# Performance work log

Measured on AMD Instinct MI355X. Metric: run time of the kernel, lower is better.

Reference implementation:

```python
import jax, jax.numpy as jnp
import numpy as np

R, K = 16, 64  # rel_size (heads), key_size (head dim)
LN_EPS = 1e-5


def apply_rope(x, pos):
    # pos: [B,S,1,K], halves are sin/cos; x: [B,S,R,K]
    sin, cos = jnp.split(pos, 2, axis=-1)
    x0, x1 = jnp.split(x, 2, axis=-1)
    return jnp.concatenate([x0 * cos - x1 * sin, x0 * sin + x1 * cos], axis=-1)


def setup_inputs() -> dict:
    key = jax.random.key(0)
    ks = jax.random.split(key, 6)
    B, S, H = 2, 2048, 1024
    x = jax.random.normal(ks[0], (B, S, H), dtype=jnp.float32)
    pos = jax.random.uniform(ks[1], (B, S, 1, K), dtype=jnp.float32)
    W_qkv = jax.random.normal(ks[2], (H, R * K * 3), dtype=jnp.float32) * (H ** -0.5)
    b_qkv = jax.random.normal(ks[3], (R * K * 3,), dtype=jnp.float32) * 0.02
    W_out = jax.random.normal(ks[4], (R * K, H), dtype=jnp.float32) * ((R * K) ** -0.5)
    b_out = jax.random.normal(ks[5], (H,), dtype=jnp.float32) * 0.02
    ln_g = jnp.ones((H,), dtype=jnp.float32)
    ln_b = jnp.zeros((H,), dtype=jnp.float32)
    return {"x": x, "pos": pos, "W_qkv": W_qkv, "b_qkv": b_qkv,
            "W_out": W_out, "b_out": b_out, "ln_g": ln_g, "ln_b": ln_b}


def reference(x, pos, W_qkv, b_qkv, W_out, b_out, ln_g, ln_b):
    B, S, H = x.shape
    qkv = (x @ W_qkv + b_qkv).reshape(B, S, R, 3 * K)
    q, k, v = jnp.split(qkv, 3, axis=-1)  # each [B,S,R,K]
    k = k / jnp.linalg.norm(k, axis=-1, keepdims=True)
    q = apply_rope(q, pos)
    k = apply_rope(k, pos)
    # SDPA with scale=1 (as in the original call)
    scores = jnp.einsum('bqhd,bkhd->bhqk', q, k)
    attn = jax.nn.softmax(scores, axis=-1)
    ctx = jnp.einsum('bhqk,bkhd->bqhd', attn, v).reshape(B, S, R * K)
    postx = ctx @ W_out + b_out
    y = x + postx
    mu = jnp.mean(y, axis=-1, keepdims=True)
    var = jnp.mean(jnp.square(y - mu), axis=-1, keepdims=True)
    return (y - mu) * jax.lax.rsqrt(var + LN_EPS) * ln_g + ln_b
```

## Files before the change

### kernel.cpp

```cpp
#include <hip/hip_runtime.h>


#define B_   2
#define S_   2048
#define H_   1024
#define R_   16
#define BS_  (B_*S_)
#define NQKV 3072
#define LOG2E 1.44269504088896f

typedef float    floatx4 __attribute__((ext_vector_type(4)));
typedef _Float16 half8   __attribute__((ext_vector_type(8)));
typedef _Float16 half4   __attribute__((ext_vector_type(4)));
typedef __fp16   fp16x2  __attribute__((ext_vector_type(2)));

#if __has_builtin(__builtin_amdgcn_exp2f)
#define EXP2(x) __builtin_amdgcn_exp2f(x)
#else
#define EXP2(x) exp2f(x)
#endif

__device__ __forceinline__ void gl_lds16(const _Float16* g, _Float16* l) {
    __builtin_amdgcn_global_load_lds(
        (const __attribute__((address_space(1))) unsigned int*)g,
        (__attribute__((address_space(3))) unsigned int*)l, 16, 0, 0);
}

__global__ __launch_bounds__(256) void cast_f16_kernel(
    const float* __restrict__ in, _Float16* __restrict__ out, int n)
{
    int i = (blockIdx.x * 256 + threadIdx.x) * 4;
    if (i >= n) return;
    float4 v = *(const float4*)(in + i);
    half4 h;
    h.x = (_Float16)v.x; h.y = (_Float16)v.y; h.z = (_Float16)v.z; h.w = (_Float16)v.w;
    *(half4*)(out + i) = h;
}

__global__ __launch_bounds__(256) void transpose_cast_f16(
    const float* __restrict__ in, _Float16* __restrict__ out, int rows, int cols)
{
    __shared__ float tile[32][33];
    int bx = blockIdx.x * 32;
    int by = blockIdx.y * 32;
    int tx = threadIdx.x & 31, ty = threadIdx.x >> 5;
#pragma unroll
    for (int i = 0; i < 32; i += 8)
        tile[ty + i][tx] = in[(size_t)(by + ty + i) * cols + bx + tx];
    __syncthreads();
#pragma unroll
    for (int i = 0; i < 32; i += 8)
        out[(size_t)(bx + ty + i) * rows + by + tx] = (_Float16)tile[tx][ty + i];
}

template <bool F16OUT>
__global__ __launch_bounds__(256) void gemm_f16_mfma(
    const _Float16* __restrict__ A, const _Float16* __restrict__ Bt,
    const float* __restrict__ bias, const float* __restrict__ resid,
    float* __restrict__ Cf, _Float16* __restrict__ Ch, int M, int N, int Kd)
{
    __shared__ _Float16 Als[2][4096];
    __shared__ _Float16 Bls[2][4096];
    int tid  = threadIdx.x;
    int lane = tid & 63, w = tid >> 6;
    int wr = w >> 1, wc = w & 1;
    int fr = lane & 15, fq = lane >> 4;
    int m0 = blockIdx.y * 128, n0 = blockIdx.x * 128;

    floatx4 acc[4][4] = {};

    const _Float16* ga[2]; const _Float16* gb[2];
    int loff[2];
#pragma unroll
    for (int i2 = 0; i2 < 2; ++i2) {
        int ch = 2 * w + i2;
        int row = ch * 16 + (lane >> 2), col = (lane & 3) * 8;
        ga[i2] = A  + (size_t)(m0 + row) * Kd + col;
        gb[i2] = Bt + (size_t)(n0 + row) * Kd + col;
        loff[i2] = ch * 512;
    }

    int nIter = Kd >> 5;
#pragma unroll
    for (int i2 = 0; i2 < 2; ++i2) {
        gl_lds16(ga[i2], &Als[0][loff[i2]]);
        gl_lds16(gb[i2], &Bls[0][loff[i2]]);
    }

    for (int it = 0; it < nIter; ++it) {
        int cur = it & 1;
        __syncthreads();
        if (it + 1 < nIter) {
            int k1 = (it + 1) << 5;
#pragma unroll
            for (int i2 = 0; i2 < 2; ++i2) {
                gl_lds16(ga[i2] + k1, &Als[cur ^ 1][loff[i2]]);
                gl_lds16(gb[i2] + k1, &Bls[cur ^ 1][loff[i2]]);
            }
        }
        const _Float16* Ab = Als[cur];
        const _Float16* Bb = Bls[cur];
        half8 af[4], bf[4];
#pragma unroll
        for (int i = 0; i < 4; ++i)
            af[i] = *(const half8*)(Ab + (wr * 64 + i * 16 + fr) * 32 + fq * 8);
#pragma unroll
        for (int j = 0; j < 4; ++j)
            bf[j] = *(const half8*)(Bb + (wc * 64 + j * 16 + fr) * 32 + fq * 8);
#pragma unroll
        for (int i = 0; i < 4; ++i)
#pragma unroll
            for (int j = 0; j < 4; ++j)
                acc[i][j] = __builtin_amdgcn_mfma_f32_16x16x32_f16(
                    af[i], bf[j], acc[i][j], 0, 0, 0);
    }

#pragma unroll
    for (int i = 0; i < 4; ++i)
#pragma unroll
        for (int j = 0; j < 4; ++j)
#pragma unroll
            for (int r2 = 0; r2 < 4; ++r2) {
                int row = m0 + wr * 64 + i * 16 + fq * 4 + r2;
                int col = n0 + wc * 64 + j * 16 + fr;
                float v = acc[i][j][r2] + bias[col];
                if constexpr (F16OUT) {
                    Ch[(size_t)row * N + col] = (_Float16)v;
                } else {
                    if (resid) v += resid[(size_t)row * N + col];
                    Cf[(size_t)row * N + col] = v;
                }
            }
}

__global__ __launch_bounds__(256) void rope_kernel(
    const _Float16* __restrict__ qkvh, const float* __restrict__ pos,
    _Float16* __restrict__ qt, _Float16* __restrict__ kt)
{
    int task = blockIdx.x * 4 + (threadIdx.x >> 6);
    int lane = threadIdx.x & 63;
    int r = task & 15, bs = task >> 4;
    int b = bs >> 11, s = bs & 2047;

    const _Float16* base = qkvh + (size_t)bs * NQKV + r * 192;
    float qv = (float)base[lane];
    float kv = (float)base[64 + lane];

    float ss = kv * kv;
#pragma unroll
    for (int off = 32; off > 0; off >>= 1) ss += __shfl_xor(ss, off);
    kv *= rsqrtf(ss);

    int j = lane & 31;
    float sn = pos[(size_t)bs * 64 + j];
    float cs = pos[(size_t)bs * 64 + 32 + j];
    float qp = __shfl_xor(qv, 32);
    float kp = __shfl_xor(kv, 32);
    float qo, ko;
    if (lane < 32) { qo = qv * cs - qp * sn; ko = kv * cs - kp * sn; }
    else           { qo = qp * sn + qv * cs; ko = kp * sn + kv * cs; }

    size_t oidx = ((size_t)(b * 16 + r) * S_ + s) * 64 + lane;
    qt[oidx] = (_Float16)(qo * LOG2E);
    kt[oidx] = (_Float16)ko;
}

__global__ __launch_bounds__(256) void vtrans_kernel(
    const _Float16* __restrict__ qkvh, _Float16* __restrict__ vt2)
{
    __shared__ float tile[64][65];
    int head = blockIdx.x, tau = blockIdx.y;
    int s0 = tau * 64;
    int b = head >> 4, rh = head & 15;
    int tx = threadIdx.x & 63, ty = threadIdx.x >> 6;
#pragma unroll
    for (int si = ty; si < 64; si += 4)
        tile[si][tx] = (float)qkvh[(size_t)(b * S_ + s0 + si) * NQKV + rh * 192 + 128 + tx];
    __syncthreads();
    int P = tx;
    int op = P >> 3;
    int hi = (P >> 2) & 1, lo = P & 3;
#pragma unroll
    for (int d = ty; d < 64; d += 4) {
        int ol = op ^ (d & 7);
        int key = 32 * (ol >> 2) + 16 * hi + 4 * (ol & 3) + lo;
        vt2[(((size_t)head * 32 + tau) * 64 + d) * 64 + P] = (_Float16)tile[key][d];
    }
}

__global__ __launch_bounds__(256) void attn_mfma_kernel(
    const _Float16* __restrict__ qt, const _Float16* __restrict__ kt,
    const _Float16* __restrict__ vt2, _Float16* __restrict__ ctx)
{
    __shared__ _Float16 Kls[64 * 64];
    __shared__ _Float16 Vls[64 * 64];

    int head = blockIdx.x, q0 = blockIdx.y * 128;
    int b = head >> 4, rh = head & 15;
    int tid = threadIdx.x, lane = tid & 63, w = tid >> 6;
    int g = lane >> 4, c = lane & 15;

    half8 qf[2][2];
    float mL[2], l_s[2] = {0.f, 0.f};
#pragma unroll
    for (int qg = 0; qg < 2; ++qg) {
        const _Float16* qp =
            qt + ((size_t)head * S_ + q0 + w * 32 + qg * 16 + c) * 64 + 8 * g;
        qf[qg][0] = *(const half8*)qp;
        qf[qg][1] = *(const half8*)(qp + 32);
        float qq = 0.f;
#pragma unroll
        for (int i = 0; i < 8; ++i) {
            float a = (float)qf[qg][0][i], b2 = (float)qf[qg][1][i];
            qq += a * a + b2 * b2;
        }
        qq += __shfl_xor(qq, 16);
        qq += __shfl_xor(qq, 32);
        mL[qg] = sqrtf(qq);
    }

    floatx4 o_acc[2][4] = {};

    const _Float16* kg[2]; const _Float16* vg[2];
    _Float16 *kl_[2], *vl_[2];
#pragma unroll
    for (int i2 = 0; i2 < 2; ++i2) {
        int ch = 2 * w + i2;
        int krow = ch * 8 + (lane >> 3);
        int koct = (lane & 7) ^ (lane >> 3);
        kg[i2] = kt + ((size_t)head * S_ + krow) * 64 + koct * 8;
        kl_[i2] = Kls + ch * 512;
        vg[i2] = vt2 + ((size_t)head * 32) * 4096 + ch * 512 + lane * 8;
        vl_[i2] = Vls + ch * 512;
    }

    int co = c & 7;

    for (int j0 = 0; j0 < S_; j0 += 64) {
        __syncthreads();
#pragma unroll
        for (int i2 = 0; i2 < 2; ++i2) {
            gl_lds16(kg[i2] + (size_t)j0 * 64, kl_[i2]);
            gl_lds16(vg[i2] + (size_t)(j0 >> 6) * 4096, vl_[i2]);
        }
        __syncthreads();

        half8 kfr[8];
#pragma unroll
        for (int t = 0; t < 4; ++t) {
            const _Float16* krow = Kls + (16 * t + c) * 64;
            kfr[2 * t]     = *(const half8*)(krow + ((g) ^ co) * 8);
            kfr[2 * t + 1] = *(const half8*)(krow + ((4 + g) ^ co) * 8);
        }

        union { half8 v; fp16x2 h2[4]; } pf[2][2];
#pragma unroll
        for (int qg = 0; qg < 2; ++qg) {
            floatx4 sacc[4];
#pragma unroll
            for (int t = 0; t < 4; ++t) {
                floatx4 z = {};
                z = __builtin_amdgcn_mfma_f32_16x16x32_f16(
                    kfr[2 * t], qf[qg][0], z, 0, 0, 0);
                z = __builtin_amdgcn_mfma_f32_16x16x32_f16(
                    kfr[2 * t + 1], qf[qg][1], z, 0, 0, 0);
                sacc[t] = z;
            }
            float mLq = mL[qg], ps = 0.f;
#pragma unroll
            for (int t = 0; t < 4; ++t)
#pragma unroll
                for (int r = 0; r < 4; ++r) {
                    float p = EXP2(sacc[t][r] - mLq);
                    sacc[t][r] = p;
                    ps += p;
                }
            l_s[qg] += ps;
            pf[qg][0].h2[0] = __builtin_amdgcn_cvt_pkrtz(sacc[0][0], sacc[0][1]);
            pf[qg][0].h2[1] = __builtin_amdgcn_cvt_pkrtz(sacc[0][2], sacc[0][3]);
            pf[qg][0].h2[2] = __builtin_amdgcn_cvt_pkrtz(sacc[1][0], sacc[1][1]);
            pf[qg][0].h2[3] = __builtin_amdgcn_cvt_pkrtz(sacc[1][2], sacc[1][3]);
            pf[qg][1].h2[0] = __builtin_amdgcn_cvt_pkrtz(sacc[2][0], sacc[2][1]);
            pf[qg][1].h2[1] = __builtin_amdgcn_cvt_pkrtz(sacc[2][2], sacc[2][3]);
            pf[qg][1].h2[2] = __builtin_amdgcn_cvt_pkrtz(sacc[3][0], sacc[3][1]);
            pf[qg][1].h2[3] = __builtin_amdgcn_cvt_pkrtz(sacc[3][2], sacc[3][3]);
        }

#pragma unroll
        for (int t = 0; t < 4; ++t) {
            const _Float16* vrow = Vls + (16 * t + c) * 64;
            half8 v0 = *(const half8*)(vrow + ((g) ^ co) * 8);
            half8 v1 = *(const half8*)(vrow + ((4 + g) ^ co) * 8);
#pragma unroll
            for (int qg = 0; qg < 2; ++qg) {
                o_acc[qg][t] = __builtin_amdgcn_mfma_f32_16x16x32_f16(
                    v0, pf[qg][0].v, o_acc[qg][t], 0, 0, 0);
                o_acc[qg][t] = __builtin_amdgcn_mfma_f32_16x16x32_f16(
                    v1, pf[qg][1].v, o_acc[qg][t], 0, 0, 0);
            }
        }
    }

#pragma unroll
    for (int qg = 0; qg < 2; ++qg) {
        float lt = l_s[qg];
        lt += __shfl_xor(lt, 16);
        lt += __shfl_xor(lt, 32);
        float inv = 1.f / lt;
        size_t rowbase =
            ((size_t)(b * S_ + q0 + w * 32 + qg * 16 + c)) * 1024 + rh * 64;
#pragma unroll
        for (int t = 0; t < 4; ++t) {
            union { half4 v; fp16x2 h2[2]; } e;
            e.h2[0] = __builtin_amdgcn_cvt_pkrtz(o_acc[qg][t][0] * inv,
                                                 o_acc[qg][t][1] * inv);
            e.h2[1] = __builtin_amdgcn_cvt_pkrtz(o_acc[qg][t][2] * inv,
                                                 o_acc[qg][t][3] * inv);
            *(half4*)(ctx + rowbase + 16 * t + 4 * g) = e.v;
        }
    }
}

__global__ __launch_bounds__(256) void ln_kernel(
    float* __restrict__ y, const float* __restrict__ g, const float* __restrict__ bb)
{
    int row = blockIdx.x, tid = threadIdx.x;
    float* p = y + (size_t)row * 1024;
    float4 v = ((const float4*)p)[tid];
    float sum = v.x + v.y + v.z + v.w;
    float sq  = v.x*v.x + v.y*v.y + v.z*v.z + v.w*v.w;
#pragma unroll
    for (int off = 32; off > 0; off >>= 1) {
        sum += __shfl_xor(sum, off);
        sq  += __shfl_xor(sq,  off);
    }
    __shared__ float rs[4], rq[4];
    int w = tid >> 6;
    if ((tid & 63) == 0) { rs[w] = sum; rq[w] = sq; }
    __syncthreads();
    sum = rs[0] + rs[1] + rs[2] + rs[3];
    sq  = rq[0] + rq[1] + rq[2] + rq[3];
    float mean = sum * (1.f / 1024.f);
    float var  = sq * (1.f / 1024.f) - mean * mean;
    float inv  = rsqrtf(var + 1e-5f);
    float4 gv = ((const float4*)g)[tid];
    float4 bv = ((const float4*)bb)[tid];
    v.x = (v.x - mean) * inv * gv.x + bv.x;
    v.y = (v.y - mean) * inv * gv.y + bv.y;
    v.z = (v.z - mean) * inv * gv.z + bv.z;
    v.w = (v.w - mean) * inv * gv.w + bv.w;
    ((float4*)p)[tid] = v;
}

extern "C" void kernel_launch(void* const* d_in, const int* in_sizes, int n_in,
                              void* d_out, int out_size, void* d_ws, size_t ws_size,
                              hipStream_t stream)
{
    const float* x     = (const float*)d_in[0];
    const float* pos   = (const float*)d_in[1];
    const float* W_qkv = (const float*)d_in[2];
    const float* b_qkv = (const float*)d_in[3];
    const float* W_out = (const float*)d_in[4];
    const float* b_out = (const float*)d_in[5];
    const float* ln_g  = (const float*)d_in[6];
    const float* ln_b  = (const float*)d_in[7];
    float* out = (float*)d_out;

    char* ws = (char*)d_ws;
    _Float16* x_h    = (_Float16*)(ws);
    _Float16* wqkv_t = (_Float16*)(ws + ((size_t)8  << 20));
    _Float16* wout_t = (_Float16*)(ws + ((size_t)14 << 20));
    _Float16* qkvh   = (_Float16*)(ws + ((size_t)16 << 20));
    _Float16* qt_h   = (_Float16*)(ws + ((size_t)40 << 20));
    _Float16* kt_h   = (_Float16*)(ws + ((size_t)48 << 20));
    _Float16* vt2_h  = (_Float16*)(ws + ((size_t)56 << 20));
    _Float16* ctx_h  = (_Float16*)(ws + ((size_t)64 << 20));

    cast_f16_kernel<<<4096, 256, 0, stream>>>(x, x_h, BS_ * H_);
    transpose_cast_f16<<<dim3(96, 32), 256, 0, stream>>>(W_qkv, wqkv_t, H_, NQKV);
    transpose_cast_f16<<<dim3(32, 32), 256, 0, stream>>>(W_out, wout_t, H_, H_);

    gemm_f16_mfma<true><<<dim3(NQKV / 128, BS_ / 128), 256, 0, stream>>>(
        x_h, wqkv_t, b_qkv, nullptr, nullptr, qkvh, BS_, NQKV, H_);

    rope_kernel<<<BS_ * R_ / 4, 256, 0, stream>>>(qkvh, pos, qt_h, kt_h);
    vtrans_kernel<<<dim3(32, 32), 256, 0, stream>>>(qkvh, vt2_h);

    attn_mfma_kernel<<<dim3(32, 16), 256, 0, stream>>>(qt_h, kt_h, vt2_h, ctx_h);

    gemm_f16_mfma<false><<<dim3(H_ / 128, BS_ / 128), 256, 0, stream>>>(
        ctx_h, wout_t, b_out, x, out, nullptr, BS_, H_, H_);

    ln_kernel<<<BS_, 256, 0, stream>>>(out, ln_g, ln_b);
}
```

Baseline: 232.4 us.

## Merge prep kernels into fewer launches and fold max subtraction into MFMA init

Combines the x cast and the two weight transpose-casts into one launch, and merges the RoPE/k-normalisation kernel with the V transpose kernel so each block handles both for one head and sequence tile. In attention, the running max is negated and used as the MFMA accumulator's initial value, which removes a subtraction per score before exp2. The intent is to cut launch overhead and per-element ALU work. The tradeoff is that the fused RoPE loop runs serially, 16 rows per wave, inside fewer blocks, which may reduce parallelism for that stage.

```diff
diff --git a/kernel.cpp b/kernel.cpp
--- a/kernel.cpp
+++ b/kernel.cpp
@@ -14,11 +14,15 @@
 typedef _Float16 half4   __attribute__((ext_vector_type(4)));
 typedef __fp16   fp16x2  __attribute__((ext_vector_type(2)));
 
+__device__ __forceinline__ float exp2_raw(float x) {
 #if __has_builtin(__builtin_amdgcn_exp2f)
-#define EXP2(x) __builtin_amdgcn_exp2f(x)
+    return __builtin_amdgcn_exp2f(x);
 #else
-#define EXP2(x) exp2f(x)
+    float r;
+    asm("v_exp_f32 %0, %1\n\ts_nop 0" : "=v"(r) : "v"(x));
+    return r;
 #endif
+}
 
 __device__ __forceinline__ void gl_lds16(const _Float16* g, _Float16* l) {
     __builtin_amdgcn_global_load_lds(
@@ -26,31 +30,41 @@
         (__attribute__((address_space(3))) unsigned int*)l, 16, 0, 0);
 }
 
-__global__ __launch_bounds__(256) void cast_f16_kernel(
-    const float* __restrict__ in, _Float16* __restrict__ out, int n)
-{
-    int i = (blockIdx.x * 256 + threadIdx.x) * 4;
-    if (i >= n) return;
-    float4 v = *(const float4*)(in + i);
-    half4 h;
-    h.x = (_Float16)v.x; h.y = (_Float16)v.y; h.z = (_Float16)v.z; h.w = (_Float16)v.w;
-    *(half4*)(out + i) = h;
-}
-
-__global__ __launch_bounds__(256) void transpose_cast_f16(
-    const float* __restrict__ in, _Float16* __restrict__ out, int rows, int cols)
+__global__ __launch_bounds__(256) void prep0_kernel(
+    const float* __restrict__ x, _Float16* __restrict__ x_h,
+    const float* __restrict__ W_qkv, _Float16* __restrict__ wqkv_t,
+    const float* __restrict__ W_out, _Float16* __restrict__ wout_t)
 {
     __shared__ float tile[32][33];
-    int bx = blockIdx.x * 32;
-    int by = blockIdx.y * 32;
-    int tx = threadIdx.x & 31, ty = threadIdx.x >> 5;
+    int bid = blockIdx.x, tid = threadIdx.x;
+    if (bid < 4096) {
+        int i = bid * 1024 + tid * 4;
+        float4 v = *(const float4*)(x + i);
+        half4 h;
+        h.x = (_Float16)v.x; h.y = (_Float16)v.y;
+        h.z = (_Float16)v.z; h.w = (_Float16)v.w;
+        *(half4*)(x_h + i) = h;
+        return;
+    }
+    const float* in; _Float16* out; int rows, cols, bx, by;
+    if (bid < 7168) {
+        int t = bid - 4096;
+        in = W_qkv; out = wqkv_t; rows = H_; cols = NQKV;
+        bx = t % 96; by = t / 96;
+    } else {
+        int t = bid - 7168;
+        in = W_out; out = wout_t; rows = H_; cols = H_;
+        bx = t & 31; by = t >> 5;
+    }
+    int cx = bx * 32, ry = by * 32;
+    int tx = tid & 31, ty = tid >> 5;
 #pragma unroll
     for (int i = 0; i < 32; i += 8)
-        tile[ty + i][tx] = in[(size_t)(by + ty + i) * cols + bx + tx];
+        tile[ty + i][tx] = in[(size_t)(ry + ty + i) * cols + cx + tx];
     __syncthreads();
 #pragma unroll
     for (int i = 0; i < 32; i += 8)
-        out[(size_t)(bx + ty + i) * rows + by + tx] = (_Float16)tile[tx][ty + i];
+        out[(size_t)(cx + ty + i) * rows + ry + tx] = (_Float16)tile[tx][ty + i];
 }
 
 template <bool F16OUT>
@@ -133,58 +147,58 @@
             }
 }
 
-__global__ __launch_bounds__(256) void rope_kernel(
+__global__ __launch_bounds__(256) void prep1_kernel(
     const _Float16* __restrict__ qkvh, const float* __restrict__ pos,
-    _Float16* __restrict__ qt, _Float16* __restrict__ kt)
-{
-    int task = blockIdx.x * 4 + (threadIdx.x >> 6);
-    int lane = threadIdx.x & 63;
-    int r = task & 15, bs = task >> 4;
-    int b = bs >> 11, s = bs & 2047;
-
-    const _Float16* base = qkvh + (size_t)bs * NQKV + r * 192;
-    float qv = (float)base[lane];
-    float kv = (float)base[64 + lane];
-
-    float ss = kv * kv;
-#pragma unroll
-    for (int off = 32; off > 0; off >>= 1) ss += __shfl_xor(ss, off);
-    kv *= rsqrtf(ss);
-
-    int j = lane & 31;
-    float sn = pos[(size_t)bs * 64 + j];
-    float cs = pos[(size_t)bs * 64 + 32 + j];
-    float qp = __shfl_xor(qv, 32);
-    float kp = __shfl_xor(kv, 32);
-    float qo, ko;
-    if (lane < 32) { qo = qv * cs - qp * sn; ko = kv * cs - kp * sn; }
-    else           { qo = qp * sn + qv * cs; ko = kp * sn + kv * cs; }
-
-    size_t oidx = ((size_t)(b * 16 + r) * S_ + s) * 64 + lane;
-    qt[oidx] = (_Float16)(qo * LOG2E);
-    kt[oidx] = (_Float16)ko;
-}
-
-__global__ __launch_bounds__(256) void vtrans_kernel(
-    const _Float16* __restrict__ qkvh, _Float16* __restrict__ vt2)
+    _Float16* __restrict__ qt, _Float16* __restrict__ kt,
+    _Float16* __restrict__ vt2)
 {
     __shared__ float tile[64][65];
     int head = blockIdx.x, tau = blockIdx.y;
     int s0 = tau * 64;
     int b = head >> 4, rh = head & 15;
-    int tx = threadIdx.x & 63, ty = threadIdx.x >> 6;
-#pragma unroll
-    for (int si = ty; si < 64; si += 4)
-        tile[si][tx] = (float)qkvh[(size_t)(b * S_ + s0 + si) * NQKV + rh * 192 + 128 + tx];
+    int lane = threadIdx.x & 63, w = threadIdx.x >> 6;
+
+#pragma unroll
+    for (int si = w; si < 64; si += 4)
+        tile[si][lane] =
+            (float)qkvh[(size_t)(b * S_ + s0 + si) * NQKV + rh * 192 + 128 + lane];
     __syncthreads();
-    int P = tx;
-    int op = P >> 3;
-    int hi = (P >> 2) & 1, lo = P & 3;
-#pragma unroll
-    for (int d = ty; d < 64; d += 4) {
-        int ol = op ^ (d & 7);
-        int key = 32 * (ol >> 2) + 16 * hi + 4 * (ol & 3) + lo;
-        vt2[(((size_t)head * 32 + tau) * 64 + d) * 64 + P] = (_Float16)tile[key][d];
+    {
+        int P = lane;
+        int op = P >> 3;
+        int hi = (P >> 2) & 1, lo = P & 3;
+#pragma unroll
+        for (int d = w; d < 64; d += 4) {
+            int ol = op ^ (d & 7);
+            int key = 32 * (ol >> 2) + 16 * hi + 4 * (ol & 3) + lo;
+            vt2[(((size_t)head * 32 + tau) * 64 + d) * 64 + P] = (_Float16)tile[key][d];
+        }
+    }
+
+    for (int i = 0; i < 16; ++i) {
+        int s = s0 + w * 16 + i;
+        int bs = b * S_ + s;
+        const _Float16* base = qkvh + (size_t)bs * NQKV + rh * 192;
+        float qv = (float)base[lane];
+        float kv = (float)base[64 + lane];
+
+        float ss = kv * kv;
+#pragma unroll
+        for (int off = 32; off > 0; off >>= 1) ss += __shfl_xor(ss, off);
+        kv *= rsqrtf(ss);
+
+        int j = lane & 31;
+        float sn = pos[(size_t)bs * 64 + j];
+        float cs = pos[(size_t)bs * 64 + 32 + j];
+        float qp = __shfl_xor(qv, 32);
+        float kp = __shfl_xor(kv, 32);
+        float qo, ko;
+        if (lane < 32) { qo = qv * cs - qp * sn; ko = kv * cs - kp * sn; }
+        else           { qo = qp * sn + qv * cs; ko = kp * sn + kv * cs; }
+
+        size_t oidx = ((size_t)head * S_ + s) * 64 + lane;
+        qt[oidx] = (_Float16)(qo * LOG2E);
+        kt[oidx] = (_Float16)ko;
     }
 }
 
@@ -256,22 +270,24 @@
         union { half8 v; fp16x2 h2[4]; } pf[2][2];
 #pragma unroll
         for (int qg = 0; qg < 2; ++qg) {
+            float negm = -mL[qg];
+            floatx4 zinit = {negm, negm, negm, negm};
             floatx4 sacc[4];
 #pragma unroll
             for (int t = 0; t < 4; ++t) {
-                floatx4 z = {};
+                floatx4 z = zinit;
                 z = __builtin_amdgcn_mfma_f32_16x16x32_f16(
                     kfr[2 * t], qf[qg][0], z, 0, 0, 0);
                 z = __builtin_amdgcn_mfma_f32_16x16x32_f16(
                     kfr[2 * t + 1], qf[qg][1], z, 0, 0, 0);
                 sacc[t] = z;
             }
-            float mLq = mL[qg], ps = 0.f;
+            float ps = 0.f;
 #pragma unroll
             for (int t = 0; t < 4; ++t)
 #pragma unroll
                 for (int r = 0; r < 4; ++r) {
-                    float p = EXP2(sacc[t][r] - mLq);
+                    float p = exp2_raw(sacc[t][r]);
                     sacc[t][r] = p;
                     ps += p;
                 }
@@ -376,15 +392,12 @@
     _Float16* vt2_h  = (_Float16*)(ws + ((size_t)56 << 20));
     _Float16* ctx_h  = (_Float16*)(ws + ((size_t)64 << 20));
 
-    cast_f16_kernel<<<4096, 256, 0, stream>>>(x, x_h, BS_ * H_);
-    transpose_cast_f16<<<dim3(96, 32), 256, 0, stream>>>(W_qkv, wqkv_t, H_, NQKV);
-    transpose_cast_f16<<<dim3(32, 32), 256, 0, stream>>>(W_out, wout_t, H_, H_);
+    prep0_kernel<<<8192, 256, 0, stream>>>(x, x_h, W_qkv, wqkv_t, W_out, wout_t);
 
     gemm_f16_mfma<true><<<dim3(NQKV / 128, BS_ / 128), 256, 0, stream>>>(
         x_h, wqkv_t, b_qkv, nullptr, nullptr, qkvh, BS_, NQKV, H_);
 
-    rope_kernel<<<BS_ * R_ / 4, 256, 0, stream>>>(qkvh, pos, qt_h, kt_h);
-    vtrans_kernel<<<dim3(32, 32), 256, 0, stream>>>(qkvh, vt2_h);
+    prep1_kernel<<<dim3(32, 32), 256, 0, stream>>>(qkvh, pos, qt_h, kt_h, vt2_h);
 
     attn_mfma_kernel<<<dim3(32, 16), 256, 0, stream>>>(qt_h, kt_h, vt2_h, ctx_h);
 
```

Result: no change. 229.4 us (-1.3%).
